# Performance work log

Measured on AMD Instinct MI355X. Metric: run time of the kernel, lower is better.

The kernel has to match this reference:

```python
import jax, jax.numpy as jnp
import numpy as np

N_NODES = 100000
N_EDGES = 1600000
DIMS = [128, 128, 128, 64]  # in, h1, h2, out


def setup_inputs() -> dict:
    key = jax.random.key(0)
    ks = jax.random.split(key, 12)
    inp = {
        "x": jax.random.normal(ks[0], (N_NODES, DIMS[0]), dtype=jnp.float32),
        "edge_index": jax.random.randint(ks[1], (2, N_EDGES), 0, N_NODES, dtype=jnp.int64),
        "edge_weights": jax.random.uniform(ks[2], (N_EDGES,), dtype=jnp.float32),
    }
    for i in range(3):
        inp[f"W{i+1}"] = jax.random.normal(ks[3 + 2 * i], (DIMS[i], DIMS[i + 1]), dtype=jnp.float32) * 0.05
        inp[f"b{i+1}"] = jax.random.normal(ks[4 + 2 * i], (DIMS[i + 1],), dtype=jnp.float32) * 0.01
    return inp


def gcn_conv(x, src, dst, w, W, b, n_nodes):
    # PyG GCNConv: linear transform, symmetric gcn_norm with self-loops (weight 1), scatter-add, bias.
    xw = x @ W                                            # [N, out]
    deg = jax.ops.segment_sum(w, dst, num_segments=n_nodes) + 1.0  # self-loop weight 1
    dinv = jnp.where(deg > 0, jax.lax.rsqrt(deg), 0.0)    # deg^{-1/2}
    norm = dinv[src] * w * dinv[dst]                      # [E]
    out = jax.ops.segment_sum(norm[:, None] * xw[src], dst, num_segments=n_nodes)
    out = out + (dinv * dinv)[:, None] * xw               # self-loop message
    return out + b


def reference(x, edge_index, edge_weights, W1, b1, W2, b2, W3, b3):
    src, dst = edge_index[0], edge_index[1]
    n = x.shape[0]
    # layer 1: GCNConv -> dropout(p=0) -> relu
    h = jax.nn.relu(gcn_conv(x, src, dst, edge_weights, W1, b1, n))
    # layer 2
    h = jax.nn.relu(gcn_conv(h, src, dst, edge_weights, W2, b2, n))
    # layer 3: activation 'none' -> Identity
    h = gcn_conv(h, src, dst, edge_weights, W3, b3, n)
    return h
```

## Files before the change

kernel.cpp:

```cpp
#include <hip/hip_runtime.h>
#include <hip/hip_fp16.h>
#include <math.h>


typedef __bf16 bf16x8 __attribute__((ext_vector_type(8)));
typedef float f32x4 __attribute__((ext_vector_type(4)));

union BF8 {
  unsigned short u[8];
  uint4 q;
  bf16x8 v;
};

__device__ __forceinline__ unsigned short rne_bf16(float f) {
  unsigned u = __float_as_uint(f);
  u += 0x7fff + ((u >> 16) & 1);
  return (unsigned short)(u >> 16);
}
__device__ __forceinline__ float bf16_to_f(unsigned short h) {
  return __uint_as_float((unsigned)h << 16);
}

__global__ __launch_bounds__(256) void edge_pass_kernel(const int* __restrict__ ei,
    const float* __restrict__ ew, unsigned long long* __restrict__ packed,
    int* __restrict__ rank, int E) {
  int e = blockIdx.x * 256 + threadIdx.x;
  if (e >= E) return;
  int d = ei[E + e];
  unsigned wfix = (unsigned)__float2uint_rn(ew[e] * 16777216.0f);
  unsigned long long inc = (1ULL << 32) | (unsigned long long)wfix;
  unsigned long long old = atomicAdd(&packed[d], inc);
  rank[e] = (int)(old >> 32);
}

__global__ __launch_bounds__(256) void dinv_kernel(const unsigned long long* __restrict__ packed,
    float* __restrict__ dinv, int n) {
  int i = blockIdx.x * 256 + threadIdx.x;
  if (i >= n) return;
  float deg = 1.0f + (float)(unsigned)(packed[i] & 0xffffffffULL) * (1.0f / 16777216.0f);
  dinv[i] = 1.0f / sqrtf(deg);
}

__global__ __launch_bounds__(1024) void scanA(const unsigned long long* __restrict__ packed,
    int* __restrict__ row_ptr, int* __restrict__ partials, int n) {
  __shared__ int sd[1024];
  int t = threadIdx.x;
  int i = blockIdx.x * 1024 + t;
  int v = (i < n) ? (int)(packed[i] >> 32) : 0;
  sd[t] = v;
  __syncthreads();
  for (int off = 1; off < 1024; off <<= 1) {
    int u = (t >= off) ? sd[t - off] : 0;
    __syncthreads();
    sd[t] += u;
    __syncthreads();
  }
  int incl = sd[t];
  if (i < n) row_ptr[i] = incl - v;
  if (t == 1023) partials[blockIdx.x] = incl;
}

__global__ __launch_bounds__(128) void scanB(int* partials, int nb) {
  __shared__ int sd[128];
  int t = threadIdx.x;
  int v = (t < nb) ? partials[t] : 0;
  sd[t] = v;
  __syncthreads();
  for (int off = 1; off < 128; off <<= 1) {
    int u = (t >= off) ? sd[t - off] : 0;
    __syncthreads();
    sd[t] += u;
    __syncthreads();
  }
  int incl = sd[t];
  partials[t] = incl - v;
  if (t == nb - 1) partials[255] = incl;
}

__global__ __launch_bounds__(1024) void scanC(int* row_ptr, const int* __restrict__ partials, int n) {
  int i = blockIdx.x * 1024 + threadIdx.x;
  if (i < n) row_ptr[i] += partials[blockIdx.x];
  if (i == 0) row_ptr[n] = partials[255];
}

__global__ __launch_bounds__(256) void fill_kernel(const int* __restrict__ ei,
    const float* __restrict__ ew, const float* __restrict__ dinv,
    const int* __restrict__ row_ptr, const int* __restrict__ rank,
    int2* __restrict__ epair, int E) {
  int e = blockIdx.x * 256 + threadIdx.x;
  if (e >= E) return;
  int s = ei[e], d = ei[E + e];
  float nw = dinv[s] * ew[e] * dinv[d];
  int p = row_ptr[d] + rank[e];
  epair[p] = make_int2(s, __float_as_int(nw));
}

template <int NCOL>
__global__ __launch_bounds__(256) void gemm_mfma_kernel(const float* __restrict__ A,
    const float* __restrict__ W, unsigned short* __restrict__ Ch, int M) {
  constexpr int NF = NCOL / 16;
  __shared__ __align__(16) unsigned short WT[2][NCOL][128];
  const int t = threadIdx.x;
  constexpr int KC_PER_IT = 256 / NCOL;
#pragma unroll
  for (int it = 0; it < 16 / KC_PER_IT; ++it) {
    int n = t % NCOL;
    int kc = it * KC_PER_IT + t / NCOL;
    int k0 = kc * 8;
    BF8 hh, ll;
#pragma unroll
    for (int j = 0; j < 8; ++j) {
      float w = W[(size_t)(k0 + j) * NCOL + n];
      unsigned short hb = rne_bf16(w);
      hh.u[j] = hb;
      ll.u[j] = rne_bf16(w - bf16_to_f(hb));
    }
    int kk = k0 ^ ((n & 7) << 3);
    *(uint4*)&WT[0][n][kk] = hh.q;
    *(uint4*)&WT[1][n][kk] = ll.q;
  }
  __syncthreads();

  const int wv = t >> 6;
  const int l = t & 63;
  const int lr = l & 15;
  const int lg = l >> 4;
  const int arow_i = blockIdx.x * 64 + wv * 16 + lr;
  const bool rv = arow_i < M;
  const float* arow = A + (size_t)arow_i * 128;

  f32x4 acc[NF] = {};
  float4 p0 = make_float4(0.f, 0.f, 0.f, 0.f), p1 = p0;
  if (rv) {
    p0 = *(const float4*)&arow[lg * 8];
    p1 = *(const float4*)&arow[lg * 8 + 4];
  }
#pragma unroll 1
  for (int ks = 0; ks < 4; ++ks) {
    int nkb = ((ks < 3) ? (ks + 1) * 32 : ks * 32) + lg * 8;
    float4 q0 = make_float4(0.f, 0.f, 0.f, 0.f), q1 = q0;
    if (rv) {
      q0 = *(const float4*)&arow[nkb];
      q1 = *(const float4*)&arow[nkb + 4];
    }
    float av[8] = {p0.x, p0.y, p0.z, p0.w, p1.x, p1.y, p1.z, p1.w};
    BF8 ah, al;
#pragma unroll
    for (int j = 0; j < 8; ++j) {
      unsigned short hb = rne_bf16(av[j]);
      ah.u[j] = hb;
      al.u[j] = rne_bf16(av[j] - bf16_to_f(hb));
    }
    int kidx = ks * 32 + lg * 8;
    BF8 bh[NF], bl[NF];
#pragma unroll
    for (int nf = 0; nf < NF; ++nf) {
      int n = nf * 16 + lr;
      int kk = kidx ^ ((n & 7) << 3);
      bh[nf].q = *(const uint4*)&WT[0][n][kk];
      bl[nf].q = *(const uint4*)&WT[1][n][kk];
    }
#pragma unroll
    for (int nf = 0; nf < NF; ++nf) {
      acc[nf] = __builtin_amdgcn_mfma_f32_16x16x32_bf16(ah.v, bh[nf].v, acc[nf], 0, 0, 0);
      acc[nf] = __builtin_amdgcn_mfma_f32_16x16x32_bf16(al.v, bh[nf].v, acc[nf], 0, 0, 0);
      acc[nf] = __builtin_amdgcn_mfma_f32_16x16x32_bf16(ah.v, bl[nf].v, acc[nf], 0, 0, 0);
    }
    p0 = q0; p1 = q1;
  }
  const int orow0 = blockIdx.x * 64 + wv * 16 + lg * 4;
#pragma unroll
  for (int j = 0; j < 4; ++j) {
    int orow = orow0 + j;
    if (orow < M) {
      unsigned short* hr = Ch + (size_t)orow * NCOL;
#pragma unroll
      for (int nf = 0; nf < NF; ++nf)
        hr[nf * 16 + lr] = __half_as_ushort(__float2half(acc[nf][j]));
    }
  }
}

template <int F, bool RELU>
__global__ __launch_bounds__(256) void agg_kernel(const unsigned short* __restrict__ xwh,
    const int* __restrict__ row_ptr, const int2* __restrict__ epair,
    const float* __restrict__ dinv, const float* __restrict__ bias,
    float* __restrict__ out, int Nn) {
  constexpr int LPN = F / 4;
  int t = blockIdx.x * 256 + threadIdx.x;
  int node = t / LPN;
  int lane = t % LPN;
  if (node >= Nn) return;
  const uint2* xh = (const uint2*)xwh;
  int start = row_ptr[node];
  int end = row_ptr[node + 1];
  float a0x = 0.f, a0y = 0.f, a0z = 0.f, a0w = 0.f;
  float a1x = 0.f, a1y = 0.f, a1z = 0.f, a1w = 0.f;
  int p = start;
  for (; p + 4 <= end; p += 4) {
    int2 e0 = epair[p];
    int2 e1 = epair[p + 1];
    int2 e2 = epair[p + 2];
    int2 e3 = epair[p + 3];
    uint2 u0 = xh[(size_t)e0.x * LPN + lane];
    uint2 u1 = xh[(size_t)e1.x * LPN + lane];
    uint2 u2 = xh[(size_t)e2.x * LPN + lane];
    uint2 u3 = xh[(size_t)e3.x * LPN + lane];
    float n0 = __int_as_float(e0.y), n1 = __int_as_float(e1.y);
    float n2 = __int_as_float(e2.y), n3 = __int_as_float(e3.y);
    float2 f0a = __half22float2(*(__half2*)&u0.x), f0b = __half22float2(*(__half2*)&u0.y);
    float2 f1a = __half22float2(*(__half2*)&u1.x), f1b = __half22float2(*(__half2*)&u1.y);
    float2 f2a = __half22float2(*(__half2*)&u2.x), f2b = __half22float2(*(__half2*)&u2.y);
    float2 f3a = __half22float2(*(__half2*)&u3.x), f3b = __half22float2(*(__half2*)&u3.y);
    a0x = fmaf(n0, f0a.x, a0x); a0y = fmaf(n0, f0a.y, a0y);
    a0z = fmaf(n0, f0b.x, a0z); a0w = fmaf(n0, f0b.y, a0w);
    a1x = fmaf(n1, f1a.x, a1x); a1y = fmaf(n1, f1a.y, a1y);
    a1z = fmaf(n1, f1b.x, a1z); a1w = fmaf(n1, f1b.y, a1w);
    a0x = fmaf(n2, f2a.x, a0x); a0y = fmaf(n2, f2a.y, a0y);
    a0z = fmaf(n2, f2b.x, a0z); a0w = fmaf(n2, f2b.y, a0w);
    a1x = fmaf(n3, f3a.x, a1x); a1y = fmaf(n3, f3a.y, a1y);
    a1z = fmaf(n3, f3b.x, a1z); a1w = fmaf(n3, f3b.y, a1w);
  }
  for (; p < end; ++p) {
    int2 pr = epair[p];
    float nw = __int_as_float(pr.y);
    uint2 u = xh[(size_t)pr.x * LPN + lane];
    float2 fa = __half22float2(*(__half2*)&u.x), fb = __half22float2(*(__half2*)&u.y);
    a0x = fmaf(nw, fa.x, a0x); a0y = fmaf(nw, fa.y, a0y);
    a0z = fmaf(nw, fb.x, a0z); a0w = fmaf(nw, fb.y, a0w);
  }
  float di = dinv[node];
  float sw = di * di;
  uint2 su = xh[(size_t)node * LPN + lane];
  float2 sa = __half22float2(*(__half2*)&su.x), sb = __half22float2(*(__half2*)&su.y);
  a0x = fmaf(sw, sa.x, a0x); a0y = fmaf(sw, sa.y, a0y);
  a0z = fmaf(sw, sb.x, a0z); a0w = fmaf(sw, sb.y, a0w);
  float4 b = ((const float4*)bias)[lane];
  float ox = a0x + a1x + b.x;
  float oy = a0y + a1y + b.y;
  float oz = a0z + a1z + b.z;
  float ow = a0w + a1w + b.w;
  if (RELU) {
    ox = fmaxf(ox, 0.f); oy = fmaxf(oy, 0.f);
    oz = fmaxf(oz, 0.f); ow = fmaxf(ow, 0.f);
  }
  ((float4*)out)[(size_t)node * LPN + lane] = make_float4(ox, oy, oz, ow);
}

extern "C" void kernel_launch(void* const* d_in, const int* in_sizes, int n_in,
                              void* d_out, int out_size, void* d_ws, size_t ws_size,
                              hipStream_t stream) {
  const float* x  = (const float*)d_in[0];
  const int*   ei = (const int*)d_in[1];
  const float* ew = (const float*)d_in[2];
  const float* W1 = (const float*)d_in[3];
  const float* b1 = (const float*)d_in[4];
  const float* W2 = (const float*)d_in[5];
  const float* b2 = (const float*)d_in[6];
  const float* W3 = (const float*)d_in[7];
  const float* b3 = (const float*)d_in[8];

  const int N = in_sizes[0] / 128;
  const int E = in_sizes[2];

  char* ws = (char*)d_ws;
  size_t off = 0;
  auto carve = [&](size_t bytes) -> void* {
    void* p = ws + off;
    off += (bytes + 255) & ~(size_t)255;
    return p;
  };
  unsigned long long* packed = (unsigned long long*)carve((size_t)N * 8);
  int*   rank    = (int*)carve((size_t)E * 4);
  float* dinv    = (float*)carve((size_t)N * 4);
  int*   row_ptr = (int*)carve((size_t)(N + 1) * 4);
  int*   parts   = (int*)carve(256 * 4);
  int2*  epair   = (int2*)carve((size_t)E * 8);
  float* bufF    = (float*)carve((size_t)N * 128 * 4);
  unsigned short* bufH = (unsigned short*)carve((size_t)N * 128 * 2);
  (void)ws_size; (void)n_in; (void)out_size;

  const int nThreads = 256;
  int gN  = (N + nThreads - 1) / nThreads;
  int gE  = (E + nThreads - 1) / nThreads;
  int nb  = (N + 1023) / 1024;

  hipMemsetAsync(packed, 0, (size_t)N * 8, stream);
  edge_pass_kernel<<<gE, nThreads, 0, stream>>>(ei, ew, packed, rank, E);
  dinv_kernel<<<gN, nThreads, 0, stream>>>(packed, dinv, N);
  scanA<<<nb, 1024, 0, stream>>>(packed, row_ptr, parts, N);
  scanB<<<1, 128, 0, stream>>>(parts, nb);
  scanC<<<nb, 1024, 0, stream>>>(row_ptr, parts, N);
  fill_kernel<<<gE, nThreads, 0, stream>>>(ei, ew, dinv, row_ptr, rank, epair, E);

  const int gMM = (N + 63) / 64;
  int gAgg128 = (N * 32 + nThreads - 1) / nThreads;
  int gAgg64  = (N * 16 + nThreads - 1) / nThreads;

  gemm_mfma_kernel<128><<<gMM, 256, 0, stream>>>(x, W1, bufH, N);
  agg_kernel<128, true><<<gAgg128, nThreads, 0, stream>>>(bufH, row_ptr, epair, dinv, b1, bufF, N);

  gemm_mfma_kernel<128><<<gMM, 256, 0, stream>>>(bufF, W2, bufH, N);
  agg_kernel<128, true><<<gAgg128, nThreads, 0, stream>>>(bufH, row_ptr, epair, dinv, b2, bufF, N);

  gemm_mfma_kernel<64><<<gMM, 256, 0, stream>>>(bufF, W3, bufH, N);
  agg_kernel<64, false><<<gAgg64, nThreads, 0, stream>>>(bufH, row_ptr, epair, dinv, b3, (float*)d_out, N);
}
```

Before: 365.7 us.

## Fuse first GEMM with edge degree pass and store hidden activations as fp16

The layer-1 GEMM and the edge degree/rank atomic pass now run in one launch, with blocks split by index, so both independent workloads share the GPU. Hidden activations between layers are written by the aggregation kernels as fp16 instead of fp32. The following GEMMs read that fp16 input, which halves the intermediate traffic. This adds rounding of activations to fp16 before the next GEMM, which lowers precision somewhat. It also makes GEMM and atomic blocks compete for resources inside the fused launch.

```diff
diff --git a/kernel.cpp b/kernel.cpp
--- a/kernel.cpp
+++ b/kernel.cpp
@@ -21,16 +21,139 @@
   return __uint_as_float((unsigned)h << 16);
 }
 
-__global__ __launch_bounds__(256) void edge_pass_kernel(const int* __restrict__ ei,
-    const float* __restrict__ ew, unsigned long long* __restrict__ packed,
-    int* __restrict__ rank, int E) {
-  int e = blockIdx.x * 256 + threadIdx.x;
-  if (e >= E) return;
-  int d = ei[E + e];
-  unsigned wfix = (unsigned)__float2uint_rn(ew[e] * 16777216.0f);
-  unsigned long long inc = (1ULL << 32) | (unsigned long long)wfix;
-  unsigned long long old = atomicAdd(&packed[d], inc);
-  rank[e] = (int)(old >> 32);
+template <int NCOL, bool AH>
+__device__ __forceinline__ void gemm_body(const void* Av, const float* __restrict__ W,
+    unsigned short* __restrict__ Ch, int M, int bid) {
+  constexpr int NF = NCOL / 16;
+  __shared__ __align__(16) unsigned short WT[2][NCOL][128];
+  const int t = threadIdx.x;
+  constexpr int KC_PER_IT = 256 / NCOL;
+#pragma unroll
+  for (int it = 0; it < 16 / KC_PER_IT; ++it) {
+    int n = t % NCOL;
+    int kc = it * KC_PER_IT + t / NCOL;
+    int k0 = kc * 8;
+    BF8 hh, ll;
+#pragma unroll
+    for (int j = 0; j < 8; ++j) {
+      float w = W[(size_t)(k0 + j) * NCOL + n];
+      unsigned short hb = rne_bf16(w);
+      hh.u[j] = hb;
+      ll.u[j] = rne_bf16(w - bf16_to_f(hb));
+    }
+    int kk = k0 ^ ((n & 7) << 3);
+    *(uint4*)&WT[0][n][kk] = hh.q;
+    *(uint4*)&WT[1][n][kk] = ll.q;
+  }
+  __syncthreads();
+
+  const int wv = t >> 6;
+  const int l = t & 63;
+  const int lr = l & 15;
+  const int lg = l >> 4;
+  const int arow_i = bid * 64 + wv * 16 + lr;
+  const bool rv = arow_i < M;
+
+  const float* arowf = (const float*)Av + (size_t)arow_i * 128;
+  const unsigned short* arowh = (const unsigned short*)Av + (size_t)arow_i * 128;
+
+  f32x4 acc[NF] = {};
+  float4 p0 = make_float4(0.f, 0.f, 0.f, 0.f), p1 = p0;
+  uint4 ph = make_uint4(0, 0, 0, 0);
+  if (rv) {
+    if constexpr (AH) {
+      ph = *(const uint4*)&arowh[lg * 8];
+    } else {
+      p0 = *(const float4*)&arowf[lg * 8];
+      p1 = *(const float4*)&arowf[lg * 8 + 4];
+    }
+  }
+#pragma unroll 1
+  for (int ks = 0; ks < 4; ++ks) {
+    int nkb = ((ks < 3) ? (ks + 1) * 32 : ks * 32) + lg * 8;
+    float4 q0 = make_float4(0.f, 0.f, 0.f, 0.f), q1 = q0;
+    uint4 qh = make_uint4(0, 0, 0, 0);
+    if (rv) {
+      if constexpr (AH) {
+        qh = *(const uint4*)&arowh[nkb];
+      } else {
+        q0 = *(const float4*)&arowf[nkb];
+        q1 = *(const float4*)&arowf[nkb + 4];
+      }
+    }
+    float av[8];
+    if constexpr (AH) {
+      union { uint4 q; __half2 h2[4]; } uu;
+      uu.q = ph;
+#pragma unroll
+      for (int j = 0; j < 4; ++j) {
+        float2 f = __half22float2(uu.h2[j]);
+        av[j * 2] = f.x; av[j * 2 + 1] = f.y;
+      }
+    } else {
+      av[0] = p0.x; av[1] = p0.y; av[2] = p0.z; av[3] = p0.w;
+      av[4] = p1.x; av[5] = p1.y; av[6] = p1.z; av[7] = p1.w;
+    }
+    BF8 ah, al;
+#pragma unroll
+    for (int j = 0; j < 8; ++j) {
+      unsigned short hb = rne_bf16(av[j]);
+      ah.u[j] = hb;
+      al.u[j] = rne_bf16(av[j] - bf16_to_f(hb));
+    }
+    int kidx = ks * 32 + lg * 8;
+    BF8 bh[NF], bl[NF];
+#pragma unroll
+    for (int nf = 0; nf < NF; ++nf) {
+      int n = nf * 16 + lr;
+      int kk = kidx ^ ((n & 7) << 3);
+      bh[nf].q = *(const uint4*)&WT[0][n][kk];
+      bl[nf].q = *(const uint4*)&WT[1][n][kk];
+    }
+#pragma unroll
+    for (int nf = 0; nf < NF; ++nf) {
+      acc[nf] = __builtin_amdgcn_mfma_f32_16x16x32_bf16(ah.v, bh[nf].v, acc[nf], 0, 0, 0);
+      acc[nf] = __builtin_amdgcn_mfma_f32_16x16x32_bf16(al.v, bh[nf].v, acc[nf], 0, 0, 0);
+      acc[nf] = __builtin_amdgcn_mfma_f32_16x16x32_bf16(ah.v, bl[nf].v, acc[nf], 0, 0, 0);
+    }
+    p0 = q0; p1 = q1; ph = qh;
+  }
+  const int orow0 = bid * 64 + wv * 16 + lg * 4;
+#pragma unroll
+  for (int j = 0; j < 4; ++j) {
+    int orow = orow0 + j;
+    if (orow < M) {
+      unsigned short* hr = Ch + (size_t)orow * NCOL;
+#pragma unroll
+      for (int nf = 0; nf < NF; ++nf)
+        hr[nf * 16 + lr] = __half_as_ushort(__float2half(acc[nf][j]));
+    }
+  }
+}
+
+__global__ __launch_bounds__(256) void pre_gemm_fused_kernel(
+    const float* __restrict__ x, const float* __restrict__ W1,
+    unsigned short* __restrict__ Ch, int M,
+    const int* __restrict__ ei, const float* __restrict__ ew,
+    unsigned long long* __restrict__ packed, int* __restrict__ rank,
+    int E, int gemmBlocks) {
+  if ((int)blockIdx.x < gemmBlocks) {
+    gemm_body<128, false>(x, W1, Ch, M, blockIdx.x);
+  } else {
+    int e = (blockIdx.x - gemmBlocks) * 256 + threadIdx.x;
+    if (e >= E) return;
+    int d = ei[E + e];
+    unsigned wfix = (unsigned)__float2uint_rn(ew[e] * 16777216.0f);
+    unsigned long long inc = (1ULL << 32) | (unsigned long long)wfix;
+    unsigned long long old = atomicAdd(&packed[d], inc);
+    rank[e] = (int)(old >> 32);
+  }
+}
+
+template <int NCOL, bool AH>
+__global__ __launch_bounds__(256) void gemm_mfma_kernel(const void* __restrict__ A,
+    const float* __restrict__ W, unsigned short* __restrict__ Ch, int M) {
+  gemm_body<NCOL, AH>(A, W, Ch, M, blockIdx.x);
 }
 
 __global__ __launch_bounds__(256) void dinv_kernel(const unsigned long long* __restrict__ packed,
@@ -95,97 +218,11 @@
   epair[p] = make_int2(s, __float_as_int(nw));
 }
 
-template <int NCOL>
-__global__ __launch_bounds__(256) void gemm_mfma_kernel(const float* __restrict__ A,
-    const float* __restrict__ W, unsigned short* __restrict__ Ch, int M) {
-  constexpr int NF = NCOL / 16;
-  __shared__ __align__(16) unsigned short WT[2][NCOL][128];
-  const int t = threadIdx.x;
-  constexpr int KC_PER_IT = 256 / NCOL;
-#pragma unroll
-  for (int it = 0; it < 16 / KC_PER_IT; ++it) {
-    int n = t % NCOL;
-    int kc = it * KC_PER_IT + t / NCOL;
-    int k0 = kc * 8;
-    BF8 hh, ll;
-#pragma unroll
-    for (int j = 0; j < 8; ++j) {
-      float w = W[(size_t)(k0 + j) * NCOL + n];
-      unsigned short hb = rne_bf16(w);
-      hh.u[j] = hb;
-      ll.u[j] = rne_bf16(w - bf16_to_f(hb));
-    }
-    int kk = k0 ^ ((n & 7) << 3);
-    *(uint4*)&WT[0][n][kk] = hh.q;
-    *(uint4*)&WT[1][n][kk] = ll.q;
-  }
-  __syncthreads();
-
-  const int wv = t >> 6;
-  const int l = t & 63;
-  const int lr = l & 15;
-  const int lg = l >> 4;
-  const int arow_i = blockIdx.x * 64 + wv * 16 + lr;
-  const bool rv = arow_i < M;
-  const float* arow = A + (size_t)arow_i * 128;
-
-  f32x4 acc[NF] = {};
-  float4 p0 = make_float4(0.f, 0.f, 0.f, 0.f), p1 = p0;
-  if (rv) {
-    p0 = *(const float4*)&arow[lg * 8];
-    p1 = *(const float4*)&arow[lg * 8 + 4];
-  }
-#pragma unroll 1
-  for (int ks = 0; ks < 4; ++ks) {
-    int nkb = ((ks < 3) ? (ks + 1) * 32 : ks * 32) + lg * 8;
-    float4 q0 = make_float4(0.f, 0.f, 0.f, 0.f), q1 = q0;
-    if (rv) {
-      q0 = *(const float4*)&arow[nkb];
-      q1 = *(const float4*)&arow[nkb + 4];
-    }
-    float av[8] = {p0.x, p0.y, p0.z, p0.w, p1.x, p1.y, p1.z, p1.w};
-    BF8 ah, al;
-#pragma unroll
-    for (int j = 0; j < 8; ++j) {
-      unsigned short hb = rne_bf16(av[j]);
-      ah.u[j] = hb;
-      al.u[j] = rne_bf16(av[j] - bf16_to_f(hb));
-    }
-    int kidx = ks * 32 + lg * 8;
-    BF8 bh[NF], bl[NF];
-#pragma unroll
-    for (int nf = 0; nf < NF; ++nf) {
-      int n = nf * 16 + lr;
-      int kk = kidx ^ ((n & 7) << 3);
-      bh[nf].q = *(const uint4*)&WT[0][n][kk];
-      bl[nf].q = *(const uint4*)&WT[1][n][kk];
-    }
-#pragma unroll
-    for (int nf = 0; nf < NF; ++nf) {
-      acc[nf] = __builtin_amdgcn_mfma_f32_16x16x32_bf16(ah.v, bh[nf].v, acc[nf], 0, 0, 0);
-      acc[nf] = __builtin_amdgcn_mfma_f32_16x16x32_bf16(al.v, bh[nf].v, acc[nf], 0, 0, 0);
-      acc[nf] = __builtin_amdgcn_mfma_f32_16x16x32_bf16(ah.v, bl[nf].v, acc[nf], 0, 0, 0);
-    }
-    p0 = q0; p1 = q1;
-  }
-  const int orow0 = blockIdx.x * 64 + wv * 16 + lg * 4;
-#pragma unroll
-  for (int j = 0; j < 4; ++j) {
-    int orow = orow0 + j;
-    if (orow < M) {
-      unsigned short* hr = Ch + (size_t)orow * NCOL;
-#pragma unroll
-      for (int nf = 0; nf < NF; ++nf)
-        hr[nf * 16 + lr] = __half_as_ushort(__float2half(acc[nf][j]));
-    }
-  }
-}
-
-template <int F, bool RELU>
+template <int F, bool RELU, bool OUTF16>
 __global__ __launch_bounds__(256) void agg_kernel(const unsigned short* __restrict__ xwh,
     const int* __restrict__ row_ptr, const int2* __restrict__ epair,
     const float* __restrict__ dinv, const float* __restrict__ bias,
-    float* __restrict__ out, int Nn) {
+    void* __restrict__ out, int Nn) {
   constexpr int LPN = F / 4;
   int t = blockIdx.x * 256 + threadIdx.x;
   int node = t / LPN;
@@ -244,7 +281,16 @@
     ox = fmaxf(ox, 0.f); oy = fmaxf(oy, 0.f);
     oz = fmaxf(oz, 0.f); ow = fmaxf(ow, 0.f);
   }
-  ((float4*)out)[(size_t)node * LPN + lane] = make_float4(ox, oy, oz, ow);
+  if constexpr (OUTF16) {
+    uint2 o;
+    __half2 h0 = __float22half2_rn(make_float2(ox, oy));
+    __half2 h1 = __float22half2_rn(make_float2(oz, ow));
+    o.x = *reinterpret_cast<unsigned*>(&h0);
+    o.y = *reinterpret_cast<unsigned*>(&h1);
+    ((uint2*)out)[(size_t)node * LPN + lane] = o;
+  } else {
+    ((float4*)out)[(size_t)node * LPN + lane] = make_float4(ox, oy, oz, ow);
+  }
 }
 
 extern "C" void kernel_launch(void* const* d_in, const int* in_sizes, int n_in,
@@ -276,33 +322,33 @@
   int*   row_ptr = (int*)carve((size_t)(N + 1) * 4);
   int*   parts   = (int*)carve(256 * 4);
   int2*  epair   = (int2*)carve((size_t)E * 8);
-  float* bufF    = (float*)carve((size_t)N * 128 * 4);
   unsigned short* bufH = (unsigned short*)carve((size_t)N * 128 * 2);
+  unsigned short* bufI = (unsigned short*)carve((size_t)N * 128 * 2);
   (void)ws_size; (void)n_in; (void)out_size;
 
   const int nThreads = 256;
   int gN  = (N + nThreads - 1) / nThreads;
   int gE  = (E + nThreads - 1) / nThreads;
   int nb  = (N + 1023) / 1024;
+  const int gMM = (N + 63) / 64;
+  int gAgg128 = (N * 32 + nThreads - 1) / nThreads;
+  int gAgg64  = (N * 16 + nThreads - 1) / nThreads;
 
   hipMemsetAsync(packed, 0, (size_t)N * 8, stream);
-  edge_pass_kernel<<<gE, nThreads, 0, stream>>>(ei, ew, packed, rank, E);
+  pre_gemm_fused_kernel<<<gMM + gE, nThreads, 0, stream>>>(
+      x, W1, bufH, N, ei, ew, packed, rank, E, gMM);
+
   dinv_kernel<<<gN, nThreads, 0, stream>>>(packed, dinv, N);
   scanA<<<nb, 1024, 0, stream>>>(packed, row_ptr, parts, N);
   scanB<<<1, 128, 0, stream>>>(parts, nb);
   scanC<<<nb, 1024, 0, stream>>>(row_ptr, parts, N);
   fill_kernel<<<gE, nThreads, 0, stream>>>(ei, ew, dinv, row_ptr, rank, epair, E);
 
-  const int gMM = (N + 63) / 64;
-  int gAgg128 = (N * 32 + nThreads - 1) / nThreads;
-  int gAgg64  = (N * 16 + nThreads - 1) / nThreads;
-
-  gemm_mfma_kernel<128><<<gMM, 256, 0, stream>>>(x, W1, bufH, N);
-  agg_kernel<128, true><<<gAgg128, nThreads, 0, stream>>>(bufH, row_ptr, epair, dinv, b1, bufF, N);
-
-  gemm_mfma_kernel<128><<<gMM, 256, 0, stream>>>(bufF, W2, bufH, N);
-  agg_kernel<128, true><<<gAgg128, nThreads, 0, stream>>>(bufH, row_ptr, epair, dinv, b2, bufF, N);
-
-  gemm_mfma_kernel<64><<<gMM, 256, 0, stream>>>(bufF, W3, bufH, N);
-  agg_kernel<64, false><<<gAgg64, nThreads, 0, stream>>>(bufH, row_ptr, epair, dinv, b3, (float*)d_out, N);
-}
+  agg_kernel<128, true, true><<<gAgg128, nThreads, 0, stream>>>(bufH, row_ptr, epair, dinv, b1, bufI, N);
+
+  gemm_mfma_kernel<128, true><<<gMM, nThreads, 0, stream>>>(bufI, W2, bufH, N);
+  agg_kernel<128, true, true><<<gAgg128, nThreads, 0, stream>>>(bufH, row_ptr, epair, dinv, b2, bufI, N);
+
+  gemm_mfma_kernel<64, true><<<gMM, nThreads, 0, stream>>>(bufI, W3, bufH, N);
+  agg_kernel<64, false, false><<<gAgg64, nThreads, 0, stream>>>(bufH, row_ptr, epair, dinv, b3, d_out, N);
+}
```

Result: faster. 347.9 us (-4.9%).
